# Kernel tuning notes

Measured on AMD Instinct MI355X. Metric: run time of the kernel, lower is better.

Reference implementation:

```python
import jax, jax.numpy as jnp
import numpy as np

B, I, H, DEPTH = 128, 768, 768, 8        # levels 0 (root) .. 7 (leaves)
NODES = 2 ** DEPTH - 1                    # 255 nodes, heap / level order
EPS = 1e-5                                # torch LayerNorm default


def setup_inputs() -> dict:
    key = jax.random.key(0)
    ks = jax.random.split(key, 8)
    s = 0.02  # xavier-ish scale to keep gates in a sane range
    return {
        "x": jax.random.normal(ks[0], (B, NODES, I), jnp.float32),
        "Wioux": jax.random.normal(ks[1], (DEPTH, 3 * H, I), jnp.float32) * s,
        "b_ioux": jnp.zeros((DEPTH, 3 * H), jnp.float32),
        "Wiouh": jax.random.normal(ks[2], (DEPTH, 3 * H, H), jnp.float32) * s,
        "Wfx": jax.random.normal(ks[3], (DEPTH, H, I), jnp.float32) * s,
        "b_fx": jnp.ones((DEPTH, H), jnp.float32),  # fx.bias init to ones per _init_weights
        "Wfh": jax.random.normal(ks[4], (DEPTH, H, H), jnp.float32) * s,
        "b_fh": jnp.zeros((DEPTH, H), jnp.float32),
        "ln_c_g": jnp.ones((DEPTH, H), jnp.float32),
        "ln_c_b": jnp.zeros((DEPTH, H), jnp.float32),
        "ln_h_g": jnp.ones((DEPTH, H), jnp.float32),
        "ln_h_b": jnp.zeros((DEPTH, H), jnp.float32),
        "Wout": jax.random.normal(ks[5], (H, H), jnp.float32) * s,
        "b_out": jnp.zeros((H,), jnp.float32),
    }


def _ln(v, g, b):
    m = v.mean(-1, keepdims=True)
    var = ((v - m) ** 2).mean(-1, keepdims=True)
    return (v - m) / jnp.sqrt(var + EPS) * g + b


def reference(x, Wioux, b_ioux, Wiouh, Wfx, b_fx, Wfh, b_fh,
              ln_c_g, ln_c_b, ln_h_g, ln_h_b, Wout, b_out):
    """Child-Sum TreeLSTM over a complete binary tree (heap-ordered nodes),
    processed bottom-up level-by-level; depth-l nodes use parameter set l."""
    bsz = x.shape[0]
    h = None
    for l in range(DEPTH - 1, -1, -1):       # leaves -> root
        n = 2 ** l
        xs = x[:, n - 1:2 * n - 1]            # [B, n, I] inputs at level l
        iou = jnp.einsum('bni,gi->bng', xs, Wioux[l]) + b_ioux[l]
        if h is not None:
            ch_h = h.reshape(bsz, n, 2, H)    # two children per node
            iou = iou + jnp.einsum('bnh,gh->bng', ch_h.sum(2), Wiouh[l])
        i_, o_, u_ = jnp.split(iou, 3, axis=-1)
        i_ = jax.nn.sigmoid(i_)
        o_ = jax.nn.sigmoid(o_)
        u_ = jnp.tanh(u_)
        c = i_ * u_
        if h is not None:
            fxo = jnp.einsum('bni,hi->bnh', xs, Wfx[l]) + b_fx[l]
            f = jax.nn.sigmoid(fxo[:, :, None, :]
                               + jnp.einsum('bnkh,gh->bnkg', ch_h, Wfh[l]) + b_fh[l])
            # NOTE: faithful to source: f gates multiply child *hidden* states
            c = c + (f * ch_h).sum(2)
        c = _ln(c, ln_c_g[l], ln_c_b[l])
        h = o_ * jnp.tanh(c)
        h = _ln(h, ln_h_g[l], ln_h_b[l])      # dropout is identity in eval
    h_root = h[:, 0]                          # [B, H]
    return jnp.einsum('bh,gh->bg', h_root, Wout) + b_out + x[:, 0]
```

## Files before the change

### kernel.cpp

```cpp
#include <hip/hip_runtime.h>
#include <hip/hip_bf16.h>


#define Hdim 768

typedef __hip_bfloat16 bf16;
typedef __attribute__((ext_vector_type(8))) short short8;
typedef __attribute__((ext_vector_type(4))) float floatx4;

__device__ inline float b2f(unsigned short u) {
    union { unsigned int i; float f; } v; v.i = ((unsigned int)u) << 16; return v.f;
}
__device__ inline float b2f(bf16 h) { return b2f(*(unsigned short*)&h); }
__device__ inline unsigned short f2bu(float f) {
    bf16 h = __float2bfloat16(f);
    return *(unsigned short*)&h;
}
__device__ inline ushort4 cvt4(float4 v) {
    ushort4 o; o.x = f2bu(v.x); o.y = f2bu(v.y); o.z = f2bu(v.z); o.w = f2bu(v.w);
    return o;
}

__global__ __launch_bounds__(384) void conv_wcat(
    const float* __restrict__ Wioux, const float* __restrict__ Wiouh,
    const float* __restrict__ Wfx, bf16* __restrict__ W_cat)
{
    const int row = blockIdx.x;
    const int l = row / 3072;
    const int g = row % 3072;
    const int t = threadIdx.x;
    const int k2 = t << 2;
    float4 v;
    if (g < 2304) {
        const float* src = (k2 < 768)
            ? Wioux + ((long)l * 2304 + g) * 768 + k2
            : Wiouh + ((long)l * 2304 + g) * 768 + (k2 - 768);
        v = *(const float4*)src;
    } else if (k2 < 768) {
        v = *(const float4*)(Wfx + ((long)l * 768 + (g - 2304)) * 768 + k2);
    } else {
        v = make_float4(0.f, 0.f, 0.f, 0.f);
    }
    ((ushort4*)(W_cat + (long)row * 1536))[t] = cvt4(v);
}

__global__ __launch_bounds__(256) void prep_misc(
    const float* __restrict__ Wfh, const float* __restrict__ Wout,
    const float* __restrict__ b_ioux, const float* __restrict__ b_fx,
    const float* __restrict__ x,
    bf16* __restrict__ Wfh_bf, bf16* __restrict__ Wout_bf,
    float* __restrict__ b_cat, bf16* __restrict__ leafA)
{
    const int id = blockIdx.x;
    const int t = threadIdx.x;
    if (id < 4608) {
        const long i = (long)id * 256 + t;
        ((ushort4*)Wfh_bf)[i] = cvt4(((const float4*)Wfh)[i]);
    } else if (id < 5184) {
        const long i = (long)(id - 4608) * 256 + t;
        ((ushort4*)Wout_bf)[i] = cvt4(((const float4*)Wout)[i]);
    } else if (id < 5280) {
        const int i = (id - 5184) * 256 + t;
        const int l = i / 3072, g = i % 3072;
        b_cat[i] = (g < 2304) ? b_ioux[l * 2304 + g] : b_fx[l * 768 + (g - 2304)];
    } else if (t < 192) {
        const int m = id - 5280;
        const int b = m >> 7, j = m & 127;
        const float* xr = x + ((long)b * 255 + 127 + j) * Hdim;
        ((ushort4*)(leafA + (long)m * Hdim))[t] = cvt4(((const float4*)xr)[t]);
    }
}

struct GemmDesc {
    const bf16* A; int lda;
    const bf16* W; int ldw;
    const float* bias;
    void* C; int ldc; int c_fp32;
    int K; int nxb;
    const float* addv; long add_stride;
};

__global__ __launch_bounds__(256) void gemm_dual(GemmDesc da, int na, GemmDesc db)
{
    __shared__ __align__(16) bf16 As[128 * 32];
    __shared__ __align__(16) bf16 Ws[128 * 32];
    int id = blockIdx.x;
    const bool second = (id >= na);
    if (second) id -= na;
    const GemmDesc d = second ? db : da;
    const int bm = id / d.nxb, bn = id % d.nxb;

    const int t = threadIdx.x;
    const int wave = t >> 6, lane = t & 63;
    const long m_blk = (long)bm << 7;
    const long n_blk = (long)bn << 7;

    const int srow = (wave << 5) + (lane >> 2);
    const int sbyte = (lane & 3) << 4;
    const char* gA = (const char*)(d.A + (m_blk + srow) * (long)d.lda) + sbyte;
    const char* gW = (const char*)(d.W + (n_blk + srow) * (long)d.ldw) + sbyte;
    const long aRow16 = (long)d.lda * 32;
    const long wRow16 = (long)d.ldw * 32;
    bf16* lA = As + (wave << 10);
    bf16* lW = Ws + (wave << 10);

    floatx4 zero = {0.f, 0.f, 0.f, 0.f};
    floatx4 acc[4][4];
#pragma unroll
    for (int i = 0; i < 4; i++)
#pragma unroll
        for (int j = 0; j < 4; j++) acc[i][j] = zero;

    const int mrow = (wave & 1) << 6;
    const int ncol = (wave >> 1) << 6;
    const short* AsS = (const short*)As;
    const short* WsS = (const short*)Ws;
    const int fm = lane & 15;
    const int fk = (lane >> 4) << 3;

    for (int k0 = 0; k0 < d.K; k0 += 32) {
        __builtin_amdgcn_global_load_lds(
            (const __attribute__((address_space(1))) unsigned int*)gA,
            (__attribute__((address_space(3))) unsigned int*)lA, 16, 0, 0);
        __builtin_amdgcn_global_load_lds(
            (const __attribute__((address_space(1))) unsigned int*)(gA + aRow16),
            (__attribute__((address_space(3))) unsigned int*)(lA + 512), 16, 0, 0);
        __builtin_amdgcn_global_load_lds(
            (const __attribute__((address_space(1))) unsigned int*)gW,
            (__attribute__((address_space(3))) unsigned int*)lW, 16, 0, 0);
        __builtin_amdgcn_global_load_lds(
            (const __attribute__((address_space(1))) unsigned int*)(gW + wRow16),
            (__attribute__((address_space(3))) unsigned int*)(lW + 512), 16, 0, 0);
        gA += 64; gW += 64;
        __syncthreads();

        short8 af[4], bfr[4];
#pragma unroll
        for (int i = 0; i < 4; i++) {
            af[i]  = *(const short8*)(AsS + (mrow + i * 16 + fm) * 32 + fk);
            bfr[i] = *(const short8*)(WsS + (ncol + i * 16 + fm) * 32 + fk);
        }
#pragma unroll
        for (int i = 0; i < 4; i++)
#pragma unroll
            for (int j = 0; j < 4; j++)
                acc[i][j] = __builtin_amdgcn_mfma_f32_16x16x32_bf16(
                    af[i], bfr[j], acc[i][j], 0, 0, 0);
        __syncthreads();
    }

    const int crow0 = (lane >> 4) << 2;
    const int ccol = lane & 15;
#pragma unroll
    for (int i = 0; i < 4; i++) {
#pragma unroll
        for (int j = 0; j < 4; j++) {
            const long col = n_blk + ncol + j * 16 + ccol;
            const float bv = d.bias ? d.bias[col] : 0.f;
#pragma unroll
            for (int r = 0; r < 4; r++) {
                const long row = m_blk + mrow + i * 16 + crow0 + r;
                float v = acc[i][j][r] + bv;
                if (d.addv) v += d.addv[row * d.add_stride + col];
                if (d.c_fp32) ((float*)d.C)[row * (long)d.ldc + col] = v;
                else ((bf16*)d.C)[row * (long)d.ldc + col] = __float2bfloat16(v);
            }
        }
    }
}

static inline GemmDesc mkdesc(const bf16* A, int lda, const bf16* W, int ldw,
                              const float* bias, void* C, int ldc, int c_fp32,
                              int K, int nxb, const float* addv, long add_stride) {
    GemmDesc d; d.A = A; d.lda = lda; d.W = W; d.ldw = ldw; d.bias = bias;
    d.C = C; d.ldc = ldc; d.c_fp32 = c_fp32; d.K = K; d.nxb = nxb;
    d.addv = addv; d.add_stride = add_stride; return d;
}

__device__ inline float sigf(float x) { return 1.f / (1.f + __expf(-x)); }
__device__ inline float tanh_fast(float x) { return 2.f / (1.f + __expf(-2.f * x)) - 1.f; }

__device__ inline void block_reduce4(float& a, float& b, float& c, float& d,
                                     float* s) {
#pragma unroll
    for (int off = 32; off > 0; off >>= 1) {
        a += __shfl_down(a, off, 64);
        b += __shfl_down(b, off, 64);
        c += __shfl_down(c, off, 64);
        d += __shfl_down(d, off, 64);
    }
    const int lane = threadIdx.x & 63, w = threadIdx.x >> 6;
    __syncthreads();
    if (lane == 0) { s[w] = a; s[w + 4] = b; s[w + 8] = c; s[w + 12] = d; }
    __syncthreads();
    a = s[0] + s[1] + s[2] + s[3];
    b = s[4] + s[5] + s[6] + s[7];
    c = s[8] + s[9] + s[10] + s[11];
    d = s[12] + s[13] + s[14] + s[15];
}

__global__ __launch_bounds__(256) void pointwise_pair(
    const bf16* __restrict__ C, int ldc,
    const bf16* __restrict__ fhb,
    const bf16* __restrict__ hprev2,
    const float* __restrict__ x,
    const float* __restrict__ bfh,
    const float* __restrict__ gc, const float* __restrict__ bc,
    const float* __restrict__ gh, const float* __restrict__ bh,
    bf16* __restrict__ hout,
    bf16* __restrict__ Anext,
    int m0, int lp)
{
    __shared__ float sred[16];
    const int pl = blockIdx.x;
    const bf16* cr0 = C + (long)(2 * pl) * ldc;
    const bf16* cr1 = cr0 + ldc;
    float c0v[3], c1v[3], o0v[3], o1v[3], h0v[3], h1v[3];
    float s0 = 0.f, q0 = 0.f, s1 = 0.f, q1 = 0.f;
#pragma unroll
    for (int tI = 0; tI < 3; tI++) {
        const int j = threadIdx.x + tI * 256;
        const float i0 = sigf(b2f(cr0[j]));
        const float i1 = sigf(b2f(cr1[j]));
        o0v[tI] = b2f(cr0[Hdim + j]);
        o1v[tI] = b2f(cr1[Hdim + j]);
        float c0 = i0 * tanh_fast(b2f(cr0[2 * Hdim + j]));
        float c1 = i1 * tanh_fast(b2f(cr1[2 * Hdim + j]));
        if (fhb) {
            const float bfhj = bfh[j];
            const float fx0 = b2f(cr0[3 * Hdim + j]);
            const float fx1 = b2f(cr1[3 * Hdim + j]);
            const long base = (long)(4 * pl) * Hdim + j;
            const float f00 = sigf(fx0 + b2f(fhb[base]) + bfhj);
            const float f01 = sigf(fx0 + b2f(fhb[base + Hdim]) + bfhj);
            const float f10 = sigf(fx1 + b2f(fhb[base + 2 * Hdim]) + bfhj);
            const float f11 = sigf(fx1 + b2f(fhb[base + 3 * Hdim]) + bfhj);
            c0 += f00 * b2f(hprev2[base]) + f01 * b2f(hprev2[base + Hdim]);
            c1 += f10 * b2f(hprev2[base + 2 * Hdim]) + f11 * b2f(hprev2[base + 3 * Hdim]);
        }
        c0v[tI] = c0; c1v[tI] = c1;
        s0 += c0; q0 += c0 * c0; s1 += c1; q1 += c1 * c1;
    }
    block_reduce4(s0, q0, s1, q1, sred);
    const float m0c = s0 / Hdim, m1c = s1 / Hdim;
    const float r0c = rsqrtf(q0 / Hdim - m0c * m0c + 1e-5f);
    const float r1c = rsqrtf(q1 / Hdim - m1c * m1c + 1e-5f);
    float hs0 = 0.f, hq0 = 0.f, hs1 = 0.f, hq1 = 0.f;
#pragma unroll
    for (int tI = 0; tI < 3; tI++) {
        const int j = threadIdx.x + tI * 256;
        const float cn0 = (c0v[tI] - m0c) * r0c * gc[j] + bc[j];
        const float cn1 = (c1v[tI] - m1c) * r1c * gc[j] + bc[j];
        const float h0 = sigf(o0v[tI]) * tanh_fast(cn0);
        const float h1 = sigf(o1v[tI]) * tanh_fast(cn1);
        h0v[tI] = h0; h1v[tI] = h1;
        hs0 += h0; hq0 += h0 * h0; hs1 += h1; hq1 += h1 * h1;
    }
    block_reduce4(hs0, hq0, hs1, hq1, sred);
    const float mh0 = hs0 / Hdim, mh1 = hs1 / Hdim;
    const float rh0 = rsqrtf(hq0 / Hdim - mh0 * mh0 + 1e-5f);
    const float rh1 = rsqrtf(hq1 / Hdim - mh1 * mh1 + 1e-5f);

    const int pg = m0 / 2 + pl;
    const int b = pg >> lp;
    const int jn = pg & ((1 << lp) - 1);
    const float* xr = x + ((long)b * 255 + (1 << lp) - 1 + jn) * Hdim;
    bf16* arow = Anext + (long)pg * 1536;
#pragma unroll
    for (int tI = 0; tI < 3; tI++) {
        const int j = threadIdx.x + tI * 256;
        const float h0 = (h0v[tI] - mh0) * rh0 * gh[j] + bh[j];
        const float h1 = (h1v[tI] - mh1) * rh1 * gh[j] + bh[j];
        hout[(long)(2 * pl) * Hdim + j] = __float2bfloat16(h0);
        hout[(long)(2 * pl + 1) * Hdim + j] = __float2bfloat16(h1);
        arow[768 + j] = __float2bfloat16(h0 + h1);
        arow[j] = __float2bfloat16(xr[j]);
    }
}

__global__ __launch_bounds__(256) void pointwise_root(
    const bf16* __restrict__ C, int ldc,
    const bf16* __restrict__ fhb, const bf16* __restrict__ hprev,
    const float* __restrict__ bfh,
    const float* __restrict__ gc, const float* __restrict__ bc,
    const float* __restrict__ gh, const float* __restrict__ bh,
    bf16* __restrict__ hout)
{
    __shared__ float sred[16];
    const int m = blockIdx.x;
    const bf16* cr = C + (long)m * ldc;
    float cv[3], ov[3], hv[3];
    float ssum = 0.f, ssq = 0.f, d0 = 0.f, d1 = 0.f;
#pragma unroll
    for (int tI = 0; tI < 3; tI++) {
        const int j = threadIdx.x + tI * 256;
        const float i_ = sigf(b2f(cr[j]));
        ov[tI] = b2f(cr[Hdim + j]);
        float c = i_ * tanh_fast(b2f(cr[2 * Hdim + j]));
        const float fx = b2f(cr[3 * Hdim + j]);
        const float bfhj = bfh[j];
        const long base = (long)(2 * m) * Hdim + j;
        const float f0 = sigf(fx + b2f(fhb[base]) + bfhj);
        const float f1 = sigf(fx + b2f(fhb[base + Hdim]) + bfhj);
        c += f0 * b2f(hprev[base]) + f1 * b2f(hprev[base + Hdim]);
        cv[tI] = c; ssum += c; ssq += c * c;
    }
    block_reduce4(ssum, ssq, d0, d1, sred);
    const float mean = ssum / Hdim;
    const float rstd = rsqrtf(ssq / Hdim - mean * mean + 1e-5f);
    float hs = 0.f, hq = 0.f;
#pragma unroll
    for (int tI = 0; tI < 3; tI++) {
        const int j = threadIdx.x + tI * 256;
        const float cn = (cv[tI] - mean) * rstd * gc[j] + bc[j];
        const float h = sigf(ov[tI]) * tanh_fast(cn);
        hv[tI] = h; hs += h; hq += h * h;
    }
    d0 = 0.f; d1 = 0.f;
    block_reduce4(hs, hq, d0, d1, sred);
    const float mh = hs / Hdim;
    const float rh = rsqrtf(hq / Hdim - mh * mh + 1e-5f);
#pragma unroll
    for (int tI = 0; tI < 3; tI++) {
        const int j = threadIdx.x + tI * 256;
        hout[(long)m * Hdim + j] = __float2bfloat16((hv[tI] - mh) * rh * gh[j] + bh[j]);
    }
}

extern "C" void kernel_launch(void* const* d_in, const int* in_sizes, int n_in,
                              void* d_out, int out_size, void* d_ws, size_t ws_size,
                              hipStream_t stream) {
    (void)in_sizes; (void)n_in; (void)out_size; (void)ws_size;
    const float* x      = (const float*)d_in[0];
    const float* Wioux  = (const float*)d_in[1];
    const float* b_ioux = (const float*)d_in[2];
    const float* Wiouh  = (const float*)d_in[3];
    const float* Wfx    = (const float*)d_in[4];
    const float* b_fx   = (const float*)d_in[5];
    const float* Wfh    = (const float*)d_in[6];
    const float* b_fh   = (const float*)d_in[7];
    const float* ln_c_g = (const float*)d_in[8];
    const float* ln_c_b = (const float*)d_in[9];
    const float* ln_h_g = (const float*)d_in[10];
    const float* ln_h_b = (const float*)d_in[11];
    const float* Wout   = (const float*)d_in[12];
    const float* b_out  = (const float*)d_in[13];
    float* out = (float*)d_out;

    char* p = (char*)d_ws;
    bf16* W_cat   = (bf16*)p; p += 8L * 3072 * 1536 * 2;
    bf16* Wfh_bf  = (bf16*)p; p += 8L * 768 * 768 * 2;
    bf16* Wout_bf = (bf16*)p; p += 768L * 768 * 2;
    float* b_cat  = (float*)p; p += 8L * 3072 * 4;
    bf16* leafA   = (bf16*)p; p += 16384L * 768 * 2;
    bf16* A6      = (bf16*)p; p += 8192L * 1536 * 2;
    bf16* A5      = (bf16*)p; p += 4096L * 1536 * 2;
    bf16* Cbuf    = (bf16*)p; p += 4096L * 3072 * 2;
    bf16* hA      = (bf16*)p; p += 16384L * 768 * 2;
    bf16* hB      = (bf16*)p; p += 8192L * 768 * 2;
    bf16* fhb     = leafA;

    conv_wcat<<<8 * 3072, 384, 0, stream>>>(Wioux, Wiouh, Wfx, W_cat);
    prep_misc<<<5280 + 16384, 256, 0, stream>>>(
        Wfh, Wout, b_ioux, b_fx, x, Wfh_bf, Wout_bf, b_cat, leafA);

    const int CH = 4096;
    GemmDesc dummy = mkdesc(nullptr, 0, nullptr, 0, nullptr, nullptr, 0, 0, 0, 1,
                            nullptr, 0);

    for (int c = 0; c < 4; c++) {
        const int m0 = c * CH;
        GemmDesc d = mkdesc(leafA + (long)m0 * 768, 768,
                            W_cat + 7L * 3072 * 1536, 1536, b_cat + 7 * 3072,
                            Cbuf, 2304, 0, 768, 18, nullptr, 0);
        gemm_dual<<<18 * (CH / 128), 256, 0, stream>>>(d, 18 * (CH / 128), dummy);
        pointwise_pair<<<CH / 2, 256, 0, stream>>>(
            Cbuf, 2304, nullptr, nullptr, x, nullptr,
            ln_c_g + 7 * Hdim, ln_c_b + 7 * Hdim, ln_h_g + 7 * Hdim, ln_h_b + 7 * Hdim,
            hA + (long)m0 * Hdim, A6, m0, 6);
    }

    bf16* hp = hA; bf16* hc = hB;
    bf16* Acur = A6; bf16* Anxt = A5;
    for (int l = 6; l >= 1; l--) {
        const int M = 128 << l;
        const int Mc = (M < CH) ? M : CH;
        const int nch = M / Mc;
        for (int c = 0; c < nch; c++) {
            const int m0 = c * Mc;
            GemmDesc diou = mkdesc(Acur + (long)m0 * 1536, 1536,
                                   W_cat + (long)l * 3072 * 1536, 1536,
                                   b_cat + l * 3072, Cbuf, 3072, 0, 1536, 24,
                                   nullptr, 0);
            GemmDesc dfh = mkdesc(hp + (long)2 * m0 * Hdim, 768,
                                  Wfh_bf + (long)l * 768 * 768, 768, nullptr,
                                  fhb, 768, 0, 768, 6, nullptr, 0);
            const int na = 24 * (Mc / 128);
            const int nb = 6 * (2 * Mc / 128);
            gemm_dual<<<na + nb, 256, 0, stream>>>(diou, na, dfh);
            pointwise_pair<<<Mc / 2, 256, 0, stream>>>(
                Cbuf, 3072, fhb, hp + (long)2 * m0 * Hdim, x, b_fh + l * Hdim,
                ln_c_g + l * Hdim, ln_c_b + l * Hdim, ln_h_g + l * Hdim, ln_h_b + l * Hdim,
                hc + (long)m0 * Hdim, Anxt, m0, l - 1);
        }
        bf16* t1 = hp; hp = hc; hc = t1;
        bf16* t2 = Acur; Acur = Anxt; Anxt = t2;
    }

    {
        GemmDesc diou = mkdesc(Acur, 1536, W_cat, 1536, b_cat, Cbuf, 3072, 0,
                               1536, 24, nullptr, 0);
        GemmDesc dfh = mkdesc(hp, 768, Wfh_bf, 768, nullptr, fhb, 768, 0,
                              768, 6, nullptr, 0);
        gemm_dual<<<24 + 12, 256, 0, stream>>>(diou, 24, dfh);
        pointwise_root<<<128, 256, 0, stream>>>(
            Cbuf, 3072, fhb, hp, b_fh,
            ln_c_g, ln_c_b, ln_h_g, ln_h_b, hc);
    }

    {
        GemmDesc dout = mkdesc(hc, 768, Wout_bf, 768, b_out, out, 768, 1,
                               768, 6, x, 255L * 768);
        gemm_dual<<<6, 256, 0, stream>>>(dout, 6, dummy);
    }
}
```

Before: 1.061 ms.

## Add 256x256-tile 8-wave MFMA GEMM with direct-to-LDS loads for tree levels

Adds a new GEMM kernel for the leaf and level 6..1 matmuls. It uses 256x256 output tiles, 8 waves and K-steps of 64, streams tiles with global_load_lds into swizzled, double-buffered LDS, interleaves loads with MFMA phases using priorities and barriers, and remaps blocks across XCDs. The leaf GEMM now runs in two 8192-row chunks, writing into an aliased A5/Cbuf region. The aim is more data reuse and higher MFMA utilisation. The risk is very few blocks at shallow levels and only one 128KB-LDS block per CU.

```diff
diff --git a/kernel.cpp b/kernel.cpp
--- a/kernel.cpp
+++ b/kernel.cpp
@@ -80,6 +80,14 @@
     const float* addv; long add_stride;
 };
 
+static inline GemmDesc mkdesc(const bf16* A, int lda, const bf16* W, int ldw,
+                              const float* bias, void* C, int ldc, int c_fp32,
+                              int K, int nxb, const float* addv, long add_stride) {
+    GemmDesc d; d.A = A; d.lda = lda; d.W = W; d.ldw = ldw; d.bias = bias;
+    d.C = C; d.ldc = ldc; d.c_fp32 = c_fp32; d.K = K; d.nxb = nxb;
+    d.addv = addv; d.add_stride = add_stride; return d;
+}
+
 __global__ __launch_bounds__(256) void gemm_dual(GemmDesc da, int na, GemmDesc db)
 {
     __shared__ __align__(16) bf16 As[128 * 32];
@@ -169,12 +177,192 @@
     }
 }
 
-static inline GemmDesc mkdesc(const bf16* A, int lda, const bf16* W, int ldw,
-                              const float* bias, void* C, int ldc, int c_fp32,
-                              int K, int nxb, const float* addv, long add_stride) {
-    GemmDesc d; d.A = A; d.lda = lda; d.W = W; d.ldw = ldw; d.bias = bias;
-    d.C = C; d.ldc = ldc; d.c_fp32 = c_fp32; d.K = K; d.nxb = nxb;
-    d.addv = addv; d.add_stride = add_stride; return d;
+__global__ __launch_bounds__(512, 2) void gemm8_dual(GemmDesc da, int na, GemmDesc db)
+{
+    __shared__ __align__(16) char smem[131072];
+
+    int id = blockIdx.x;
+    int nwg = na;
+    bool second = false;
+    if (id >= na) { id -= na; nwg = (int)gridDim.x - na; second = true; }
+    const GemmDesc d = second ? db : da;
+    {
+        const int q = nwg >> 3, r = nwg & 7;
+        const int x = id & 7, i2 = id >> 3;
+        id = (x < r ? x * (q + 1) : r * (q + 1) + (x - r) * q) + i2;
+    }
+    const int bm = id / d.nxb, bn = id % d.nxb;
+    const int tid = threadIdx.x;
+    const int w = tid >> 6, lane = tid & 63;
+    const long m_blk = (long)bm << 8;
+    const long n_blk = (long)bn << 8;
+    const int T = d.K >> 6;
+
+    const int colb = ((lane & 7) << 4) ^ (lane & 32);
+    const int rw = (w << 4) + (lane >> 3);
+    const long ldaB = (long)d.lda * 2, ldwB = (long)d.ldw * 2;
+    const char* gA0 = (const char*)(d.A + m_blk * d.lda) + (long)rw * ldaB + colb;
+    const char* gB0 = (const char*)(d.W + n_blk * d.ldw) + (long)rw * ldwB + colb;
+    const long aH = ldaB << 7, bH = ldwB << 7;
+    const long a8 = ldaB << 3, b8 = ldwB << 3;
+    char* lW = smem + (w << 11);
+
+    auto stageA = [&](int tile, int buf, int half) {
+        const char* g = gA0 + (half ? aH : 0) + ((long)tile << 7);
+        char* l = lW + buf * 32768 + half * 16384;
+        __builtin_amdgcn_global_load_lds(
+            (const __attribute__((address_space(1))) unsigned int*)g,
+            (__attribute__((address_space(3))) unsigned int*)l, 16, 0, 0);
+        __builtin_amdgcn_global_load_lds(
+            (const __attribute__((address_space(1))) unsigned int*)(g + a8),
+            (__attribute__((address_space(3))) unsigned int*)(l + 1024), 16, 0, 0);
+    };
+    auto stageB = [&](int tile, int buf, int half) {
+        const char* g = gB0 + (half ? bH : 0) + ((long)tile << 7);
+        char* l = lW + 65536 + buf * 32768 + half * 16384;
+        __builtin_amdgcn_global_load_lds(
+            (const __attribute__((address_space(1))) unsigned int*)g,
+            (__attribute__((address_space(3))) unsigned int*)l, 16, 0, 0);
+        __builtin_amdgcn_global_load_lds(
+            (const __attribute__((address_space(1))) unsigned int*)(g + b8),
+            (__attribute__((address_space(3))) unsigned int*)(l + 1024), 16, 0, 0);
+    };
+
+    const int fm = lane & 15;
+    const int fkB = (lane >> 4) << 4;
+    const int sx = (lane & 4) << 3;
+    const int arow0 = ((w >> 2) << 7) + fm;
+    const int brow0 = ((w & 3) << 6) + fm;
+
+    floatx4 acc[8][4];
+    const floatx4 fzero = {0.f, 0.f, 0.f, 0.f};
+#pragma unroll
+    for (int i = 0; i < 8; i++)
+#pragma unroll
+        for (int j = 0; j < 4; j++) acc[i][j] = fzero;
+
+    stageA(0, 0, 0); stageA(0, 0, 1); stageB(0, 0, 0); stageB(0, 0, 1);
+    if (T > 1) {
+        stageB(1, 1, 0); stageB(1, 1, 1); stageA(1, 1, 0);
+        asm volatile("s_waitcnt vmcnt(6)" ::: "memory");
+    } else {
+        asm volatile("s_waitcnt vmcnt(0)" ::: "memory");
+    }
+    __builtin_amdgcn_sched_barrier(0);
+    __builtin_amdgcn_s_barrier();
+    __builtin_amdgcn_sched_barrier(0);
+
+    short8 a[4][2], b[4][2];
+    for (int tt = 0; tt < T; ++tt) {
+        const int buf = tt & 1;
+        const char* la = smem + buf * 32768;
+        const char* lb = smem + 65536 + buf * 32768;
+#pragma unroll
+        for (int mf = 0; mf < 4; ++mf)
+#pragma unroll
+            for (int ks = 0; ks < 2; ++ks)
+                a[mf][ks] = *(const short8*)(la + ((((arow0 + mf * 16) << 7) + ks * 64 + fkB) ^ sx));
+#pragma unroll
+        for (int nf = 0; nf < 2; ++nf)
+#pragma unroll
+            for (int ks = 0; ks < 2; ++ks)
+                b[nf][ks] = *(const short8*)(lb + ((((brow0 + nf * 16) << 7) + ks * 64 + fkB) ^ sx));
+        if (tt + 1 < T) stageA(tt + 1, buf ^ 1, 1);
+        __builtin_amdgcn_s_barrier();
+        asm volatile("s_waitcnt lgkmcnt(0)" ::: "memory");
+        __builtin_amdgcn_sched_barrier(0);
+        __builtin_amdgcn_s_setprio(1);
+#pragma unroll
+        for (int ks = 0; ks < 2; ++ks)
+#pragma unroll
+            for (int mf = 0; mf < 4; ++mf)
+#pragma unroll
+                for (int nf = 0; nf < 2; ++nf)
+                    acc[mf][nf] = __builtin_amdgcn_mfma_f32_16x16x32_bf16(
+                        a[mf][ks], b[nf][ks], acc[mf][nf], 0, 0, 0);
+        __builtin_amdgcn_s_setprio(0);
+        __builtin_amdgcn_s_barrier();
+        __builtin_amdgcn_sched_barrier(0);
+#pragma unroll
+        for (int nf = 0; nf < 2; ++nf)
+#pragma unroll
+            for (int ks = 0; ks < 2; ++ks)
+                b[2 + nf][ks] = *(const short8*)(lb + ((((brow0 + (2 + nf) * 16) << 7) + ks * 64 + fkB) ^ sx));
+        __builtin_amdgcn_s_barrier();
+        asm volatile("s_waitcnt lgkmcnt(0)" ::: "memory");
+        __builtin_amdgcn_sched_barrier(0);
+        __builtin_amdgcn_s_setprio(1);
+#pragma unroll
+        for (int ks = 0; ks < 2; ++ks)
+#pragma unroll
+            for (int mf = 0; mf < 4; ++mf)
+#pragma unroll
+                for (int nf = 0; nf < 2; ++nf)
+                    acc[mf][2 + nf] = __builtin_amdgcn_mfma_f32_16x16x32_bf16(
+                        a[mf][ks], b[2 + nf][ks], acc[mf][2 + nf], 0, 0, 0);
+        __builtin_amdgcn_s_setprio(0);
+        __builtin_amdgcn_s_barrier();
+        __builtin_amdgcn_sched_barrier(0);
+#pragma unroll
+        for (int mf = 0; mf < 4; ++mf)
+#pragma unroll
+            for (int ks = 0; ks < 2; ++ks)
+                a[mf][ks] = *(const short8*)(la + ((((arow0 + (4 + mf) * 16) << 7) + ks * 64 + fkB) ^ sx));
+        if (tt + 2 < T) stageB(tt + 2, buf, 0);
+        __builtin_amdgcn_s_barrier();
+        asm volatile("s_waitcnt lgkmcnt(0)" ::: "memory");
+        __builtin_amdgcn_sched_barrier(0);
+        __builtin_amdgcn_s_setprio(1);
+#pragma unroll
+        for (int ks = 0; ks < 2; ++ks)
+#pragma unroll
+            for (int mf = 0; mf < 4; ++mf)
+#pragma unroll
+                for (int nf = 0; nf < 2; ++nf)
+                    acc[4 + mf][2 + nf] = __builtin_amdgcn_mfma_f32_16x16x32_bf16(
+                        a[mf][ks], b[2 + nf][ks], acc[4 + mf][2 + nf], 0, 0, 0);
+        __builtin_amdgcn_s_setprio(0);
+        __builtin_amdgcn_s_barrier();
+        __builtin_amdgcn_sched_barrier(0);
+        if (tt + 2 < T) { stageB(tt + 2, buf, 1); stageA(tt + 2, buf, 0); }
+        __builtin_amdgcn_s_setprio(1);
+#pragma unroll
+        for (int ks = 0; ks < 2; ++ks)
+#pragma unroll
+            for (int mf = 0; mf < 4; ++mf)
+#pragma unroll
+                for (int nf = 0; nf < 2; ++nf)
+                    acc[4 + mf][nf] = __builtin_amdgcn_mfma_f32_16x16x32_bf16(
+                        a[mf][ks], b[nf][ks], acc[4 + mf][nf], 0, 0, 0);
+        __builtin_amdgcn_s_setprio(0);
+        if (tt + 1 < T) {
+            if (tt + 2 < T) asm volatile("s_waitcnt vmcnt(6)" ::: "memory");
+            else            asm volatile("s_waitcnt vmcnt(0)" ::: "memory");
+            __builtin_amdgcn_sched_barrier(0);
+            __builtin_amdgcn_s_barrier();
+            __builtin_amdgcn_sched_barrier(0);
+        }
+    }
+
+    const int crow = (lane >> 4) << 2;
+    const int ccol = lane & 15;
+    const long row0 = m_blk + ((long)(w >> 2) << 7);
+    const long col0 = n_blk + ((w & 3) << 6);
+#pragma unroll
+    for (int mf = 0; mf < 8; ++mf) {
+#pragma unroll
+        for (int nf = 0; nf < 4; ++nf) {
+            const long col = col0 + nf * 16 + ccol;
+            const float bv = d.bias ? d.bias[col] : 0.f;
+#pragma unroll
+            for (int r = 0; r < 4; ++r) {
+                const long row = row0 + mf * 16 + crow + r;
+                const float v = acc[mf][nf][r] + bv;
+                if (d.c_fp32) ((float*)d.C)[row * (long)d.ldc + col] = v;
+                else ((bf16*)d.C)[row * (long)d.ldc + col] = __float2bfloat16(v);
+            }
+        }
+    }
 }
 
 __device__ inline float sigf(float x) { return 1.f / (1.f + __expf(-x)); }
@@ -359,27 +547,28 @@
     bf16* hA      = (bf16*)p; p += 16384L * 768 * 2;
     bf16* hB      = (bf16*)p; p += 8192L * 768 * 2;
     bf16* fhb     = leafA;
+    bf16* Cleaf   = A5;
 
     conv_wcat<<<8 * 3072, 384, 0, stream>>>(Wioux, Wiouh, Wfx, W_cat);
     prep_misc<<<5280 + 16384, 256, 0, stream>>>(
         Wfh, Wout, b_ioux, b_fx, x, Wfh_bf, Wout_bf, b_cat, leafA);
 
-    const int CH = 4096;
     GemmDesc dummy = mkdesc(nullptr, 0, nullptr, 0, nullptr, nullptr, 0, 0, 0, 1,
                             nullptr, 0);
 
-    for (int c = 0; c < 4; c++) {
-        const int m0 = c * CH;
-        GemmDesc d = mkdesc(leafA + (long)m0 * 768, 768,
-                            W_cat + 7L * 3072 * 1536, 1536, b_cat + 7 * 3072,
-                            Cbuf, 2304, 0, 768, 18, nullptr, 0);
-        gemm_dual<<<18 * (CH / 128), 256, 0, stream>>>(d, 18 * (CH / 128), dummy);
-        pointwise_pair<<<CH / 2, 256, 0, stream>>>(
-            Cbuf, 2304, nullptr, nullptr, x, nullptr,
+    for (int c = 0; c < 2; c++) {
+        const int m0 = c * 8192;
+        GemmDesc dl = mkdesc(leafA + (long)m0 * 768, 768,
+                             W_cat + 7L * 3072 * 1536, 1536, b_cat + 7 * 3072,
+                             Cleaf, 2304, 0, 768, 9, nullptr, 0);
+        gemm8_dual<<<9 * 32, 512, 0, stream>>>(dl, 9 * 32, dummy);
+        pointwise_pair<<<4096, 256, 0, stream>>>(
+            Cleaf, 2304, nullptr, nullptr, x, nullptr,
             ln_c_g + 7 * Hdim, ln_c_b + 7 * Hdim, ln_h_g + 7 * Hdim, ln_h_b + 7 * Hdim,
             hA + (long)m0 * Hdim, A6, m0, 6);
     }
 
+    const int CH = 4096;
     bf16* hp = hA; bf16* hc = hB;
     bf16* Acur = A6; bf16* Anxt = A5;
     for (int l = 6; l >= 1; l--) {
@@ -390,14 +579,14 @@
             const int m0 = c * Mc;
             GemmDesc diou = mkdesc(Acur + (long)m0 * 1536, 1536,
                                    W_cat + (long)l * 3072 * 1536, 1536,
-                                   b_cat + l * 3072, Cbuf, 3072, 0, 1536, 24,
+                                   b_cat + l * 3072, Cbuf, 3072, 0, 1536, 12,
                                    nullptr, 0);
             GemmDesc dfh = mkdesc(hp + (long)2 * m0 * Hdim, 768,
                                   Wfh_bf + (long)l * 768 * 768, 768, nullptr,
-                                  fhb, 768, 0, 768, 6, nullptr, 0);
-            const int na = 24 * (Mc / 128);
-            const int nb = 6 * (2 * Mc / 128);
-            gemm_dual<<<na + nb, 256, 0, stream>>>(diou, na, dfh);
+                                  fhb, 768, 0, 768, 3, nullptr, 0);
+            const int na = 12 * (Mc / 256);
+            const int nb = 3 * (2 * Mc / 256);
+            gemm8_dual<<<na + nb, 512, 0, stream>>>(diou, na, dfh);
             pointwise_pair<<<Mc / 2, 256, 0, stream>>>(
                 Cbuf, 3072, fhb, hp + (long)2 * m0 * Hdim, x, b_fh + l * Hdim,
                 ln_c_g + l * Hdim, ln_c_b + l * Hdim, ln_h_g + l * Hdim, ln_h_b + l * Hdim,
```

Measured after the change: 1.041 ms. About the same (-1.9%).
